# Optimization experiments

Hardware: AMD Instinct MI355X
Metric: run time of the kernel (lower is better)

Reference implementation:

```python
import jax, jax.numpy as jnp
import numpy as np

FEAT = 256
HID = 128
NL = 4
DIL = [1, 2, 4, 8]
T = 2048
IN_DIMS = [FEAT, HID, HID, HID]
OUT_DIMS = [HID, HID, HID, FEAT]


def setup_inputs() -> dict:
    key = jax.random.key(0)
    ks = jax.random.split(key, 64)
    inp = {"x": jax.random.normal(ks[0], (T, FEAT), dtype=jnp.float32)}
    ki = 1
    for i in range(NL):
        din, dout = IN_DIMS[i], OUT_DIMS[i]
        s = 1.0 / np.sqrt(dout)
        inp[f"Wih{i}"] = jax.random.uniform(ks[ki], (4 * dout, din), jnp.float32, -s, s); ki += 1
        inp[f"Whh{i}"] = jax.random.uniform(ks[ki], (4 * dout, dout), jnp.float32, -s, s); ki += 1
        inp[f"bih{i}"] = jax.random.uniform(ks[ki], (4 * dout,), jnp.float32, -s, s); ki += 1
        inp[f"bhh{i}"] = jax.random.uniform(ks[ki], (4 * dout,), jnp.float32, -s, s); ki += 1
        # initial states: h ~ U(0,1), c ~ N(0,1), one per dilation slot
        inp[f"h0_{i}"] = jax.random.uniform(ks[ki], (DIL[i], dout), jnp.float32); ki += 1
        inp[f"c0_{i}"] = jax.random.normal(ks[ki], (DIL[i], dout), jnp.float32); ki += 1
    return inp


def _lstm_cell(xv, h, c, Wih, Whh, bih, bhh):
    z = Wih @ xv + bih + Whh @ h + bhh          # [4*out]
    i, f, g, o = jnp.split(z, 4)
    i = jax.nn.sigmoid(i); f = jax.nn.sigmoid(f)
    g = jnp.tanh(g);       o = jax.nn.sigmoid(o)
    c2 = f * c + i * g
    h2 = o * jnp.tanh(c2)
    return h2, c2


def _forward(x, params, h0s, c0s):
    def step(carry, inp):
        Hs, Cs = carry
        j, xt = inp
        v = xt
        Hs, Cs = list(Hs), list(Cs)
        for i in range(NL):
            k = j % DIL[i]
            h, c = Hs[i][k], Cs[i][k]
            h2, c2 = _lstm_cell(v, h, c, *params[i])
            Hs[i] = Hs[i].at[k].set(h2)
            Cs[i] = Cs[i].at[k].set(c2)
            v = h2
        return (tuple(Hs), tuple(Cs)), v

    init = (tuple(h0s), tuple(c0s))
    _, out = jax.lax.scan(step, init, (jnp.arange(T), x))
    return out  # [T, FEAT]


def reference(x,
              Wih0, Whh0, bih0, bhh0,
              Wih1, Whh1, bih1, bhh1,
              Wih2, Whh2, bih2, bhh2,
              Wih3, Whh3, bih3, bhh3,
              h0_0, c0_0, h0_1, c0_1, h0_2, c0_2, h0_3, c0_3):
    params = [(Wih0, Whh0, bih0, bhh0), (Wih1, Whh1, bih1, bhh1),
              (Wih2, Whh2, bih2, bhh2), (Wih3, Whh3, bih3, bhh3)]
    h0s = [h0_0, h0_1, h0_2, h0_3]
    c0s = [c0_0, c0_1, c0_2, c0_3]
    return _forward(x, params, h0s, c0s)
```

## Files before the change

kernel.cpp:

```cpp
#include <hip/hip_runtime.h>


typedef unsigned int u32;
typedef _Float16 h2v __attribute__((ext_vector_type(2)));

#define TSTEPS 2048

#define ZX_FLOATS 1048576
#define Y0_OFF 0
#define Y1_OFF 32768
#define Y2_OFF 65536
#define HX_OFF 98304
#define PROG_OFF 163840
#define CNT_OFF 164352

#define CBAR() asm volatile("" ::: "memory")
__device__ __forceinline__ void barL() {
  asm volatile("s_waitcnt lgkmcnt(0)\ns_barrier" ::: "memory");
}
__device__ __forceinline__ float f_sig(float x) { return 1.0f / (1.0f + __expf(-x)); }
__device__ __forceinline__ float f_tanh(float x) {
  float xc = fminf(fmaxf(x, -15.0f), 15.0f);
  float e = __expf(2.0f * xc);
  return (e - 1.0f) / (e + 1.0f);
}
__device__ __forceinline__ u32 pld32(const u32* p) {
  return __hip_atomic_load((u32*)p, __ATOMIC_RELAXED, __HIP_MEMORY_SCOPE_SYSTEM);
}
__device__ __forceinline__ void pst16(u32* p, int j, float v) {
  _Float16 hv = (_Float16)v;
  u32 u = ((u32)(j + 1) << 16) | (u32)__builtin_bit_cast(unsigned short, hv);
  __hip_atomic_store(p, u, __ATOMIC_RELAXED, __HIP_MEMORY_SCOPE_SYSTEM);
}
__device__ __forceinline__ u32 pldA(const u32* p) {
  return __hip_atomic_load((u32*)p, __ATOMIC_RELAXED, __HIP_MEMORY_SCOPE_AGENT);
}
__device__ __forceinline__ void pstA16(u32* p, int j, float v) {
  _Float16 hv = (_Float16)v;
  u32 u = ((u32)(j + 1) << 16) | (u32)__builtin_bit_cast(unsigned short, hv);
  __hip_atomic_store(p, u, __ATOMIC_RELAXED, __HIP_MEMORY_SCOPE_AGENT);
}
__device__ __forceinline__ int ptag16(u32 u) { return (int)(short)(u >> 16); }
__device__ __forceinline__ _Float16 pval16(u32 u) {
  return __builtin_bit_cast(_Float16, (unsigned short)(u & 0xffffu));
}
__device__ __forceinline__ void ensure32(u32& u, const u32* p, int need, int& bud) {
  while (ptag16(u) < need) { if (--bud < 0) break; u = pld32(p); }
}
__device__ __forceinline__ void pollg32(const u32* p, int need, int& bud) {
  u32 g = pld32(p);
  while (ptag16(g) < need) { if (--bud < 0) break; g = pld32(p); }
}

__global__ __launch_bounds__(256) void zx0_kernel(
    const float* __restrict__ x, const float* __restrict__ Wih0,
    const float* __restrict__ bih0, const float* __restrict__ bhh0,
    float* __restrict__ zx) {
  __shared__ float xs[4 * 256];
  const int t = threadIdx.x;
  const int j0 = blockIdx.x * 4;
  ((float4*)xs)[t] = ((const float4*)(x + j0 * 256))[t];
  __syncthreads();
  const int r0 = t, r1 = t + 256;
  float a0[4] = {0, 0, 0, 0}, a1[4] = {0, 0, 0, 0};
  const float* w0p = Wih0 + r0 * 256;
  const float* w1p = Wih0 + r1 * 256;
#pragma unroll 8
  for (int k = 0; k < 256; k += 4) {
    float4 wa = *(const float4*)(w0p + k);
    float4 wb = *(const float4*)(w1p + k);
#pragma unroll
    for (int jj = 0; jj < 4; jj++) {
      float4 xv = *(const float4*)(xs + jj * 256 + k);
      a0[jj] += wa.x * xv.x + wa.y * xv.y + wa.z * xv.z + wa.w * xv.w;
      a1[jj] += wb.x * xv.x + wb.y * xv.y + wb.z * xv.z + wb.w * xv.w;
    }
  }
  float b0 = bih0[r0] + bhh0[r0];
  float b1 = bih0[r1] + bhh0[r1];
#pragma unroll
  for (int jj = 0; jj < 4; jj++) {
    zx[(j0 + jj) * 512 + r0] = a0[jj] + b0;
    zx[(j0 + jj) * 512 + r1] = a1[jj] + b1;
  }
}

__device__ void r0_run(int t, const float* __restrict__ Whh0,
                       const float* __restrict__ h00, const float* __restrict__ c00,
                       const float* __restrict__ zx, u32* __restrict__ y0,
                       const u32* __restrict__ y1g, float* LDS) {
  _Float16* hb16 = (_Float16*)LDS;
  const float4* hb4 = (const float4*)LDS;
  float* zbuf = LDS + 64;
  const int kh = t >> 7, cl = t & 127;
  h2v w[4][32];
#pragma unroll
  for (int r = 0; r < 4; r++)
#pragma unroll
    for (int kk = 0; kk < 64; kk += 4) {
      float4 a = *(const float4*)(Whh0 + (cl + 128 * r) * 128 + kh * 64 + kk);
      h2v t0; t0.x = (_Float16)a.x; t0.y = (_Float16)a.y;
      h2v t1; t1.x = (_Float16)a.z; t1.y = (_Float16)a.w;
      w[r][kk >> 1] = t0; w[r][(kk >> 1) + 1] = t1;
    }
  float c = 0.0f, zx4[4] = {0, 0, 0, 0};
  if (t < 128) {
    hb16[t] = (_Float16)h00[t]; c = c00[t];
#pragma unroll
    for (int r = 0; r < 4; r++) zx4[r] = zx[cl + 128 * r];
  }
  int bud = 1 << 22; int gu = 0;
  __syncthreads();
  for (int j = 0; j < TSTEPS; j++) {
    float4 hf[8];
#pragma unroll
    for (int i = 0; i < 8; i++) hf[i] = hb4[kh * 8 + i];
    const h2v* hh = (const h2v*)hf;
    float a0 = 0, a1 = 0, a2 = 0, a3 = 0;
#pragma unroll
    for (int kk = 0; kk < 32; kk++) {
      a0 = __builtin_amdgcn_fdot2(w[0][kk], hh[kk], a0, false);
      a1 = __builtin_amdgcn_fdot2(w[1][kk], hh[kk], a1, false);
      a2 = __builtin_amdgcn_fdot2(w[2][kk], hh[kk], a2, false);
      a3 = __builtin_amdgcn_fdot2(w[3][kk], hh[kk], a3, false);
    }
    if (kh) { zbuf[cl] = a0; zbuf[128 + cl] = a1; zbuf[256 + cl] = a2; zbuf[384 + cl] = a3; }
    barL();
    if (t < 128) {
      float zi = zx4[0] + a0 + zbuf[cl];
      float zf = zx4[1] + a1 + zbuf[128 + cl];
      float zg = zx4[2] + a2 + zbuf[256 + cl];
      float zo = zx4[3] + a3 + zbuf[384 + cl];
      float ig = f_sig(zi), fg = f_sig(zf), gg = f_tanh(zg), og = f_sig(zo);
      c = fg * c + ig * gg;
      float h2 = og * f_tanh(c);
      if (j + 1 < TSTEPS) {
#pragma unroll
        for (int r = 0; r < 4; r++) zx4[r] = zx[(j + 1) * 512 + cl + 128 * r];
      }
      CBAR();
      hb16[cl] = (_Float16)h2;
      pst16(y0 + (u32)(j & 255) * 128 + cl, j, h2);
    } else if (t == 128 && j >= 192 && j >= gu) {
      pollg32(y1g + (u32)((j + 64) & 255) * 128, (j + 64) - 255, bud);
      gu = j + 64;
    }
    barL();
  }
}

template <int D, int GM>
__device__ void rmid_run(int q, int t, const float* __restrict__ Wih,
                         const float* __restrict__ Whh,
                         const float* __restrict__ bih, const float* __restrict__ bhh,
                         const float* __restrict__ h0s, const float* __restrict__ c0s,
                         const u32* __restrict__ yin, u32* __restrict__ yout,
                         const u32* __restrict__ gptr, float* LDS) {
  _Float16* hb16 = (_Float16*)LDS;
  const float4* hb4 = (const float4*)LDS;
  _Float16* vb16 = (_Float16*)(LDS + 64);
  const float4* vb4 = (const float4*)(LDS + 64);
  float* zbuf = LDS + 128;
  const int kh = t >> 7, cl = t & 127;
  h2v wi[4][32], wr[4][32];
#pragma unroll
  for (int r = 0; r < 4; r++)
#pragma unroll
    for (int kk = 0; kk < 64; kk += 4) {
      float4 a = *(const float4*)(Wih + (cl + 128 * r) * 128 + kh * 64 + kk);
      h2v t0; t0.x = (_Float16)a.x; t0.y = (_Float16)a.y;
      h2v t1; t1.x = (_Float16)a.z; t1.y = (_Float16)a.w;
      wi[r][kk >> 1] = t0; wi[r][(kk >> 1) + 1] = t1;
      float4 b = *(const float4*)(Whh + (cl + 128 * r) * 128 + kh * 64 + kk);
      h2v t2; t2.x = (_Float16)b.x; t2.y = (_Float16)b.y;
      h2v t3; t3.x = (_Float16)b.z; t3.y = (_Float16)b.w;
      wr[r][kk >> 1] = t2; wr[r][(kk >> 1) + 1] = t3;
    }
  float bst4[4] = {0, 0, 0, 0};
  float c = 0.0f;
  if (t < 128) {
    hb16[t] = (_Float16)h0s[q * 128 + t]; c = c0s[q * 128 + t];
#pragma unroll
    for (int r = 0; r < 4; r++) bst4[r] = bih[cl + 128 * r] + bhh[cl + 128 * r];
  }
  int bud = 1 << 22; int gu = 0;
  u32 pf = 0, spf = 0;
  if (t < 128) {
    ensure32(pf, yin + (u32)(q & 255) * 128 + t, q + 1, bud);
    vb16[t] = pval16(pf);
  }
  __syncthreads();
  const int NS = TSTEPS / D;
  for (int s = 0; s < NS; s++) {
    const int j = q + s * D;
    float4 vf[8], hf[8];
#pragma unroll
    for (int i = 0; i < 8; i++) { vf[i] = vb4[kh * 8 + i]; hf[i] = hb4[kh * 8 + i]; }
    const h2v* vv = (const h2v*)vf;
    const h2v* hh = (const h2v*)hf;
    float a0 = 0, a1 = 0, a2 = 0, a3 = 0;
#pragma unroll
    for (int kk = 0; kk < 32; kk++) {
      a0 = __builtin_amdgcn_fdot2(wi[0][kk], vv[kk], a0, false);
      a1 = __builtin_amdgcn_fdot2(wi[1][kk], vv[kk], a1, false);
      a2 = __builtin_amdgcn_fdot2(wi[2][kk], vv[kk], a2, false);
      a3 = __builtin_amdgcn_fdot2(wi[3][kk], vv[kk], a3, false);
    }
#pragma unroll
    for (int kk = 0; kk < 32; kk++) {
      a0 = __builtin_amdgcn_fdot2(wr[0][kk], hh[kk], a0, false);
      a1 = __builtin_amdgcn_fdot2(wr[1][kk], hh[kk], a1, false);
      a2 = __builtin_amdgcn_fdot2(wr[2][kk], hh[kk], a2, false);
      a3 = __builtin_amdgcn_fdot2(wr[3][kk], hh[kk], a3, false);
    }
    if (kh) { zbuf[cl] = a0; zbuf[128 + cl] = a1; zbuf[256 + cl] = a2; zbuf[384 + cl] = a3; }
    barL();
    if (t < 128) {
      float zi = bst4[0] + a0 + zbuf[cl];
      float zf = bst4[1] + a1 + zbuf[128 + cl];
      float zg = bst4[2] + a2 + zbuf[256 + cl];
      float zo = bst4[3] + a3 + zbuf[384 + cl];
      float ig = f_sig(zi), fg = f_sig(zf), gg = f_tanh(zg), og = f_sig(zo);
      c = fg * c + ig * gg;
      float h2 = og * f_tanh(c);
      hb16[cl] = (_Float16)h2;
      pst16(yout + (u32)(j & 255) * 128 + cl, j, h2);
    } else {
      const int cl2 = t - 128;
      if (s + 1 < NS) {
        const int jn = j + D;
        ensure32(spf, yin + (u32)(jn & 255) * 128 + cl2, jn + 1, bud);
        vb16[cl2] = pval16(spf);
        spf = pld32(yin + (u32)((jn + D) & 255) * 128 + cl2);
      }
      if (GM == 1) {
        if (t == 192 && j >= 192 && j >= gu) {
          pollg32(gptr + (u32)((j + 64) & 255) * 128, (j + 64) - 255, bud);
          gu = j + 64;
        }
      } else {
        if (t >= 224 && t < 232 && (s & 31) == 0 && j >= 256)
          pollg32(gptr + (u32)(t - 224) * 64, j - 159, bud);
      }
    }
    barL();
  }
}

__device__ void r3_run(int q, int p, int t, const float* __restrict__ Wih3,
                       const float* __restrict__ Whh3,
                       const float* __restrict__ bih3, const float* __restrict__ bhh3,
                       const float* __restrict__ h03, const float* __restrict__ c03,
                       const u32* __restrict__ y2, u32* __restrict__ hx,
                       u32* __restrict__ prog, u32* __restrict__ donec,
                       float* __restrict__ out, float* LDS) {
  _Float16* hb16 = (_Float16*)LDS;
  const float4* hb4 = (const float4*)LDS;
  _Float16* vb16 = (_Float16*)(LDS + 128);
  const float4* vb4 = (const float4*)(LDS + 128);
  float* zbuf = LDS + 192;
  const int g = t >> 6, ci = t & 63;
  const int R = g * 256 + p * 64 + ci;
  h2v wh[128], wx[64];
#pragma unroll
  for (int kk = 0; kk < 256; kk += 4) {
    float4 a = *(const float4*)(Whh3 + R * 256 + kk);
    h2v t0; t0.x = (_Float16)a.x; t0.y = (_Float16)a.y;
    h2v t1; t1.x = (_Float16)a.z; t1.y = (_Float16)a.w;
    wh[kk >> 1] = t0; wh[(kk >> 1) + 1] = t1;
  }
#pragma unroll
  for (int kk = 0; kk < 128; kk += 4) {
    float4 a = *(const float4*)(Wih3 + R * 128 + kk);
    h2v t0; t0.x = (_Float16)a.x; t0.y = (_Float16)a.y;
    h2v t1; t1.x = (_Float16)a.z; t1.y = (_Float16)a.w;
    wx[kk >> 1] = t0; wx[(kk >> 1) + 1] = t1;
  }
  const float bst = bih3[R] + bhh3[R];
  float c = (t < 64) ? c03[q * 256 + p * 64 + t] : 0.0f;
  hb16[t] = (_Float16)h03[q * 256 + t];
  int bud = 1 << 22;
  const int pu = (t >= 64) ? ((t - 64) + ((t - 64) >= p * 64 ? 64 : 0)) : 0;
  u32 pf = 0;
  if (t < 128) {
    ensure32(pf, y2 + (u32)(q & 255) * 128 + t, q + 1, bud);
    vb16[t] = pval16(pf);
  }
  __syncthreads();
#pragma unroll 1
  for (int s = 0; s < 256; s++) {
    const int j = q + 8 * s;
    float acc = bst;
#pragma unroll
    for (int ch = 0; ch < 4; ch++) {
      float4 vf[4];
#pragma unroll
      for (int i = 0; i < 4; i++) vf[i] = vb4[ch * 4 + i];
      const h2v* vv = (const h2v*)vf;
#pragma unroll
      for (int kk = 0; kk < 16; kk++)
        acc = __builtin_amdgcn_fdot2(wx[ch * 16 + kk], vv[kk], acc, false);
    }
#pragma unroll
    for (int ch = 0; ch < 8; ch++) {
      float4 hf[4];
#pragma unroll
      for (int i = 0; i < 4; i++) hf[i] = hb4[ch * 4 + i];
      const h2v* hh = (const h2v*)hf;
#pragma unroll
      for (int kk = 0; kk < 16; kk++)
        acc = __builtin_amdgcn_fdot2(wh[ch * 16 + kk], hh[kk], acc, false);
    }
    zbuf[t] = acc;
    barL();
    if (t < 64) {
      float zi = zbuf[t], zf = zbuf[64 + t], zg = zbuf[128 + t], zo = zbuf[192 + t];
      float ig = f_sig(zi), fg = f_sig(zf), gg = f_tanh(zg), og = f_sig(zo);
      c = fg * c + ig * gg;
      float h2 = og * f_tanh(c);
      const int jn = j + 8;
      u32 a = 0, b2 = 0;
      if (s + 1 < 256) {
        a = pld32(y2 + (u32)(jn & 255) * 128 + t);
        b2 = pld32(y2 + (u32)(jn & 255) * 128 + t + 64);
      }
      CBAR();
      out[j * 256 + p * 64 + t] = h2;
      pstA16(hx + (u32)(j & 255) * 256 + p * 64 + t, j, h2);
      hb16[p * 64 + t] = (_Float16)h2;
      if (s + 1 < 256) {
        while (ptag16(a) < jn + 1) { if (--bud < 0) break; a = pld32(y2 + (u32)(jn & 255) * 128 + t); }
        vb16[t] = pval16(a);
        while (ptag16(b2) < jn + 1) { if (--bud < 0) break; b2 = pld32(y2 + (u32)(jn & 255) * 128 + t + 64); }
        vb16[t + 64] = pval16(b2);
      }
      if (t == 0 && p == 0) {
        pst16(prog + q * 64, j, 0.0f);
        if (s == 255) atomicAdd(donec, 1u);
      }
    } else if (s + 1 < 256) {
      const u32* pp = hx + (u32)(j & 255) * 256 + pu;
      u32 hu = pldA(pp);
      while (ptag16(hu) < j + 1) { if (--bud < 0) break; hu = pldA(pp); }
      hb16[pu] = pval16(hu);
    }
    barL();
  }
}

__device__ void keeper_run(int t, const u32* donec, float* LDS) {
  int* stop = (int*)LDS;
  if (t == 0) stop[0] = 0;
  __syncthreads();
  float r0 = (float)t * 0.001f + 1.0f, r1 = r0 + 0.5f, r2 = r0 + 1.5f, r3 = r0 + 2.5f;
  for (int it = 0; it < 20000; ++it) {
#pragma unroll
    for (int k = 0; k < 16; k++) {
      r0 = __builtin_fmaf(r0, 1.0000001f, 1e-7f);
      r1 = __builtin_fmaf(r1, 1.0000001f, 1e-7f);
      r2 = __builtin_fmaf(r2, 1.0000001f, 1e-7f);
      r3 = __builtin_fmaf(r3, 1.0000001f, 1e-7f);
    }
    asm volatile("" : "+v"(r0), "+v"(r1), "+v"(r2), "+v"(r3));
    if ((it & 15) == 0) {
      if (t == 0) stop[0] = ((int)pld32(donec) >= 8) ? 1 : 0;
      barL();
      int sv = stop[0];
      barL();
      if (sv) break;
    }
  }
  if (r0 == 1.2345e30f) ((volatile float*)LDS)[1] = r0;
}

__global__ __launch_bounds__(256, 1) void drnn_kernel(
    const float* __restrict__ Whh0, const float* __restrict__ h00, const float* __restrict__ c00,
    const float* __restrict__ Wih1, const float* __restrict__ Whh1,
    const float* __restrict__ bih1, const float* __restrict__ bhh1,
    const float* __restrict__ h01, const float* __restrict__ c01,
    const float* __restrict__ Wih2, const float* __restrict__ Whh2,
    const float* __restrict__ bih2, const float* __restrict__ bhh2,
    const float* __restrict__ h02, const float* __restrict__ c02,
    const float* __restrict__ Wih3, const float* __restrict__ Whh3,
    const float* __restrict__ bih3, const float* __restrict__ bhh3,
    const float* __restrict__ h03, const float* __restrict__ c03,
    float* __restrict__ ws, float* __restrict__ out) {
  __shared__ float LDS[704];
  __shared__ int role;
  const int b = blockIdx.x;
  const int t = threadIdx.x;
  const float* zx = ws;
  u32* base = (u32*)(ws + ZX_FLOATS);
  u32* y0 = base + Y0_OFF;
  u32* y1 = base + Y1_OFF;
  u32* y2 = base + Y2_OFF;
  u32* hx = base + HX_OFF;
  u32* prog = base + PROG_OFF;
  u32* cnt = base + CNT_OFF;

  if (b == 0) {
    r0_run(t, Whh0, h00, c00, zx, y0, y1, LDS);
    return;
  }
  if (b <= 2) {
    rmid_run<2, 1>(b - 1, t, Wih1, Whh1, bih1, bhh1, h01, c01, y0, y1, y2, LDS);
    return;
  }
  if (b <= 6) {
    rmid_run<4, 2>(b - 3, t, Wih2, Whh2, bih2, bhh2, h02, c02, y1, y2, prog, LDS);
    return;
  }
  if (t == 0) {
    unsigned xcc;
    asm volatile("s_getreg_b32 %0, hwreg(HW_REG_XCC_ID)" : "=s"(xcc));
    xcc &= 7u;
    u32 r = atomicAdd(cnt + xcc, 1u);
    role = (r < 4u) ? (int)(xcc * 4u + r) : -1;
  }
  __syncthreads();
  const int ro = role;
  if (ro >= 0)
    r3_run(ro >> 2, ro & 3, t, Wih3, Whh3, bih3, bhh3, h03, c03, y2, hx, prog,
           cnt + 8, out, LDS);
  else
    keeper_run(t, cnt + 8, LDS);
}

extern "C" void kernel_launch(void* const* d_in, const int* in_sizes, int n_in,
                              void* d_out, int out_size, void* d_ws, size_t ws_size,
                              hipStream_t stream) {
  const float* x    = (const float*)d_in[0];
  const float* Wih0 = (const float*)d_in[1];
  const float* Whh0 = (const float*)d_in[2];
  const float* bih0 = (const float*)d_in[3];
  const float* bhh0 = (const float*)d_in[4];
  const float* h00  = (const float*)d_in[5];
  const float* c00  = (const float*)d_in[6];
  const float* Wih1 = (const float*)d_in[7];
  const float* Whh1 = (const float*)d_in[8];
  const float* bih1 = (const float*)d_in[9];
  const float* bhh1 = (const float*)d_in[10];
  const float* h01  = (const float*)d_in[11];
  const float* c01  = (const float*)d_in[12];
  const float* Wih2 = (const float*)d_in[13];
  const float* Whh2 = (const float*)d_in[14];
  const float* bih2 = (const float*)d_in[15];
  const float* bhh2 = (const float*)d_in[16];
  const float* h02  = (const float*)d_in[17];
  const float* c02  = (const float*)d_in[18];
  const float* Wih3 = (const float*)d_in[19];
  const float* Whh3 = (const float*)d_in[20];
  const float* bih3 = (const float*)d_in[21];
  const float* bhh3 = (const float*)d_in[22];
  const float* h03  = (const float*)d_in[23];
  const float* c03  = (const float*)d_in[24];

  float* ws = (float*)d_ws;
  float* out = (float*)d_out;
  u32* cnt = (u32*)(ws + ZX_FLOATS) + CNT_OFF;

  hipMemsetAsync(cnt, 0, 64, stream);
  zx0_kernel<<<512, 256, 0, stream>>>(x, Wih0, bih0, bhh0, ws);
  drnn_kernel<<<256, 256, 0, stream>>>(Whh0, h00, c00,
                                       Wih1, Whh1, bih1, bhh1, h01, c01,
                                       Wih2, Whh2, bih2, bhh2, h02, c02,
                                       Wih3, Whh3, bih3, bhh3, h03, c03,
                                       ws, out);
}
```

Before: 1.620 ms.

## Pair K-halves in adjacent lanes with DPP reduce and double-buffer h in layer 0

Layer 0's recurrent matvec now puts the two K-halves of each output column in adjacent lanes, combining them with a DPP xor-1 add instead of an LDS round trip. The h vector is double-buffered in LDS, which drops one of the two barriers per timestep. All 256 threads now compute the gate math redundantly in pairs; even lanes write h locally, odd lanes publish to the global ring and poll for the downstream layer. This removes a barrier and an LDS exchange from the serial per-step critical path, at the cost of duplicated transcendental work and extra zx loads.

```diff
diff --git a/kernel.cpp b/kernel.cpp
--- a/kernel.cpp
+++ b/kernel.cpp
@@ -50,6 +50,10 @@
 __device__ __forceinline__ void pollg32(const u32* p, int need, int& bud) {
   u32 g = pld32(p);
   while (ptag16(g) < need) { if (--bud < 0) break; g = pld32(p); }
+}
+__device__ __forceinline__ float dpp_xor1_add(float x) {
+  int yi = __builtin_amdgcn_mov_dpp(__builtin_bit_cast(int, x), 0xB1, 0xF, 0xF, true);
+  return x + __builtin_bit_cast(float, yi);
 }
 
 __global__ __launch_bounds__(256) void zx0_kernel(
@@ -91,8 +95,7 @@
                        const u32* __restrict__ y1g, float* LDS) {
   _Float16* hb16 = (_Float16*)LDS;
   const float4* hb4 = (const float4*)LDS;
-  float* zbuf = LDS + 64;
-  const int kh = t >> 7, cl = t & 127;
+  const int cl = t >> 1, kh = t & 1;
   h2v w[4][32];
 #pragma unroll
   for (int r = 0; r < 4; r++)
@@ -103,18 +106,18 @@
       h2v t1; t1.x = (_Float16)a.z; t1.y = (_Float16)a.w;
       w[r][kk >> 1] = t0; w[r][(kk >> 1) + 1] = t1;
     }
-  float c = 0.0f, zx4[4] = {0, 0, 0, 0};
-  if (t < 128) {
-    hb16[t] = (_Float16)h00[t]; c = c00[t];
-#pragma unroll
-    for (int r = 0; r < 4; r++) zx4[r] = zx[cl + 128 * r];
-  }
+  float c = c00[cl];
+  float zx4[4];
+#pragma unroll
+  for (int r = 0; r < 4; r++) zx4[r] = zx[cl + 128 * r];
+  if (kh == 0) hb16[cl] = (_Float16)h00[cl];
   int bud = 1 << 22; int gu = 0;
   __syncthreads();
   for (int j = 0; j < TSTEPS; j++) {
+    const float4* hbr = hb4 + (j & 1) * 16;
     float4 hf[8];
 #pragma unroll
-    for (int i = 0; i < 8; i++) hf[i] = hb4[kh * 8 + i];
+    for (int i = 0; i < 8; i++) hf[i] = hbr[kh * 8 + i];
     const h2v* hh = (const h2v*)hf;
     float a0 = 0, a1 = 0, a2 = 0, a3 = 0;
 #pragma unroll
@@ -124,26 +127,28 @@
       a2 = __builtin_amdgcn_fdot2(w[2][kk], hh[kk], a2, false);
       a3 = __builtin_amdgcn_fdot2(w[3][kk], hh[kk], a3, false);
     }
-    if (kh) { zbuf[cl] = a0; zbuf[128 + cl] = a1; zbuf[256 + cl] = a2; zbuf[384 + cl] = a3; }
-    barL();
-    if (t < 128) {
-      float zi = zx4[0] + a0 + zbuf[cl];
-      float zf = zx4[1] + a1 + zbuf[128 + cl];
-      float zg = zx4[2] + a2 + zbuf[256 + cl];
-      float zo = zx4[3] + a3 + zbuf[384 + cl];
-      float ig = f_sig(zi), fg = f_sig(zf), gg = f_tanh(zg), og = f_sig(zo);
-      c = fg * c + ig * gg;
-      float h2 = og * f_tanh(c);
-      if (j + 1 < TSTEPS) {
-#pragma unroll
-        for (int r = 0; r < 4; r++) zx4[r] = zx[(j + 1) * 512 + cl + 128 * r];
-      }
-      CBAR();
-      hb16[cl] = (_Float16)h2;
+    a0 = dpp_xor1_add(a0); a1 = dpp_xor1_add(a1);
+    a2 = dpp_xor1_add(a2); a3 = dpp_xor1_add(a3);
+    float zi = zx4[0] + a0;
+    float zf = zx4[1] + a1;
+    float zg = zx4[2] + a2;
+    float zo = zx4[3] + a3;
+    float ig = f_sig(zi), fg = f_sig(zf), gg = f_tanh(zg), og = f_sig(zo);
+    c = fg * c + ig * gg;
+    float h2 = og * f_tanh(c);
+    if (j + 1 < TSTEPS) {
+#pragma unroll
+      for (int r = 0; r < 4; r++) zx4[r] = zx[(j + 1) * 512 + cl + 128 * r];
+    }
+    CBAR();
+    if (kh == 0) {
+      hb16[((j + 1) & 1) * 128 + cl] = (_Float16)h2;
+    } else {
       pst16(y0 + (u32)(j & 255) * 128 + cl, j, h2);
-    } else if (t == 128 && j >= 192 && j >= gu) {
-      pollg32(y1g + (u32)((j + 64) & 255) * 128, (j + 64) - 255, bud);
-      gu = j + 64;
+      if (t == 1 && j >= 192 && j >= gu) {
+        pollg32(y1g + (u32)((j + 64) & 255) * 128, (j + 64) - 255, bud);
+        gu = j + 64;
+      }
     }
     barL();
   }
```

Result: slower. 1.880 ms (+16.1%).
